# Performance work log

Hardware: AMD Instinct MI355X
Metric: run time of the kernel (lower is better)

## Reference

```python
import jax, jax.numpy as jnp
import numpy as np

HIDDEN = 64
DEPTH = 4  # 4 tanh layers + final linear


def _mlp(x, Ws, bs):
    # x: [..., 3] -> [..., 1]; weights stored as (in, out)
    h = x
    for W, b in zip(Ws[:-1], bs[:-1]):
        h = jnp.tanh(h @ W + b)
    return h @ Ws[-1] + bs[-1]


def setup_inputs() -> dict:
    key = jax.random.key(0)
    N = 262144
    dims = [3, HIDDEN, HIDDEN, HIDDEN, HIDDEN, 1]
    ks = jax.random.split(key, 2 * len(dims) + 3)
    inp = {}
    inp["x_data"] = jax.random.normal(ks[0], (N, 3), dtype=jnp.float32)
    inp["y_data"] = jax.random.normal(ks[1], (N, 1), dtype=jnp.float32)
    inp["x_phys"] = jax.random.normal(ks[2], (N, 3), dtype=jnp.float32)
    for i in range(5):
        fan_in = dims[i]
        bound = 1.0 / np.sqrt(fan_in)
        inp[f"W{i}"] = jax.random.uniform(ks[3 + 2 * i], (dims[i], dims[i + 1]),
                                          minval=-bound, maxval=bound, dtype=jnp.float32)
        inp[f"b{i}"] = jax.random.uniform(ks[4 + 2 * i], (dims[i + 1],),
                                          minval=-bound, maxval=bound, dtype=jnp.float32)
    inp["log_lambda"] = jnp.array([-2.0], dtype=jnp.float32)
    inp["log_alpha"] = jnp.array([-4.0], dtype=jnp.float32)
    return inp


def reference(x_data, y_data, x_phys,
              W0, b0, W1, b1, W2, b2, W3, b3, W4, b4,
              log_lambda, log_alpha):
    Ws = (W0, W1, W2, W3, W4)
    bs = (b0, b1, b2, b3, b4)
    alpha = jnp.exp(log_alpha)[0]
    lam = jnp.exp(log_lambda)[0]

    # data loss
    y_pred = _mlp(x_data, Ws, bs)  # [N,1]
    data_loss = jnp.mean((y_pred - y_data) ** 2)

    # PDE residual: dT/dt - alpha * (d2T/dx2 + d2T/dy2)
    def scalar_net(x):  # x: [3] -> scalar
        return _mlp(x, Ws, bs)[0]

    g = jax.grad(scalar_net)
    grads = jax.vmap(g)(x_phys)  # [N,3]
    dT_dt = grads[:, 2]

    e0 = jnp.array([1.0, 0.0, 0.0], dtype=x_phys.dtype)
    e1 = jnp.array([0.0, 1.0, 0.0], dtype=x_phys.dtype)

    def second_xy(x):
        # forward-over-reverse: Hessian columns for x and y directions
        _, hx = jax.jvp(g, (x,), (e0,))
        _, hy = jax.jvp(g, (x,), (e1,))
        return hx[0], hy[1]

    d2T_dx2, d2T_dy2 = jax.vmap(second_xy)(x_phys)  # each [N]

    residual = dT_dt - alpha * (d2T_dx2 + d2T_dy2)
    pde_loss = jnp.mean(residual ** 2)
    total_loss = data_loss + lam * pde_loss
    return total_loss, data_loss, pde_loss, alpha, lam
```

## Files before the change

### kernel.cpp

```cpp
#include <hip/hip_runtime.h>
#include <math.h>

#define NSAMP 262144
#define NW 8
#define BLK 512
#define GRID 1024
#define TOTW (GRID * NW)

#define SB_MASK 0x120

typedef _Float16 f16x8 __attribute__((ext_vector_type(8)));
typedef __fp16   fp16x2 __attribute__((ext_vector_type(2)));
typedef float    f32x4 __attribute__((ext_vector_type(4)));
typedef float    f32x2 __attribute__((ext_vector_type(2)));
typedef unsigned int u32;

#define PCH 4

#define TWO_LOG2E 2.8853900817779268f

union BFrag { f16x8 v[2]; u32 d[8]; };

__device__ __forceinline__ f32x2 lo2(f32x4 v) { return __builtin_shufflevector(v, v, 0, 1); }
__device__ __forceinline__ f32x2 hi2(f32x4 v) { return __builtin_shufflevector(v, v, 2, 3); }
__device__ __forceinline__ f32x2 splat2(float s) { f32x2 v; v.x = s; v.y = s; return v; }

__device__ __forceinline__ u32 pkdw(f32x2 p) {
    union { fp16x2 h; u32 u; } c;
    c.h = __builtin_amdgcn_cvt_pkrtz(p.x, p.y);
    return c.u;
}

__device__ __forceinline__ f32x2 fast_tanh2(f32x2 x) {
    f32x2 t = x * splat2(TWO_LOG2E);
    f32x2 e;
    e.x = __builtin_amdgcn_exp2f(t.x);
    e.y = __builtin_amdgcn_exp2f(t.y);
    f32x2 d = e + splat2(1.0f);
    f32x2 rc;
    rc.x = __builtin_amdgcn_rcpf(d.x);
    rc.y = __builtin_amdgcn_rcpf(d.y);
    return splat2(1.0f) - splat2(2.0f) * rc;
}

__device__ __forceinline__ void phys_half(f32x2 z0, f32x2 z1, f32x2 z2, f32x2 z3,
                                          f32x2 alpha2, f32x2 (&h)[PCH])
{
    f32x2 a    = fast_tanh2(z0);
    f32x2 ap   = splat2(1.0f) - a * a;
    f32x2 napp = (a * ap) * alpha2;
    h[0] = a;
    h[1] = ap * z1;
    h[2] = ap * z2;
    f32x2 s = z1 * z1 + z2 * z2;
    h[3] = ap * z3 + napp * s;
}

__device__ __forceinline__ f32x2 phys_resid(f32x2 z0, f32x2 z1, f32x2 z2, f32x2 z3,
                                            f32x2 alpha2)
{
    f32x2 a    = fast_tanh2(z0);
    f32x2 ap   = splat2(1.0f) - a * a;
    f32x2 napp = (a * ap) * alpha2;
    f32x2 s = z1 * z1 + z2 * z2;
    return ap * z3 + napp * s;
}

__device__ __forceinline__ double shfl_xor_d(double v, int m) {
    union { double d; int i[2]; } u; u.d = v;
    u.i[0] = __shfl_xor(u.i[0], m, 64);
    u.i[1] = __shfl_xor(u.i[1], m, 64);
    return u.d;
}

template<bool DATA, int CH>
__device__ __forceinline__ void pw_store(const f32x4* acc, BFrag (&bout)[CH],
                                         int rt, f32x2 alpha2)
{
    if constexpr (DATA) {
        #pragma unroll
        for (int c = 0; c < CH; c++) {
            bout[c].d[rt * 2 + 0] = pkdw(fast_tanh2(lo2(acc[c])));
            bout[c].d[rt * 2 + 1] = pkdw(fast_tanh2(hi2(acc[c])));
        }
    } else {
        f32x2 hlo[PCH], hhi[PCH];
        phys_half(lo2(acc[0]), lo2(acc[1]), lo2(acc[2]), lo2(acc[3]), alpha2, hlo);
        phys_half(hi2(acc[0]), hi2(acc[1]), hi2(acc[2]), hi2(acc[3]), alpha2, hhi);
        #pragma unroll
        for (int c = 0; c < CH; c++) {
            bout[c].d[rt * 2 + 0] = pkdw(hlo[c]);
            bout[c].d[rt * 2 + 1] = pkdw(hhi[c]);
        }
    }
}

template<bool DATA, int CH>
__device__ __forceinline__ void layer_mfma(
    const _Float16* sWA, const float (*sB)[64],
    int l, int rt, int q, int n, const BFrag (&bf)[CH], f32x4 (&acc)[CH])
{
    const f32x4 z4 = {0.f, 0.f, 0.f, 0.f};
    f16x8 a0k = *(const f16x8*)&sWA[((((l * 4 + rt) * 2 + 0) * 4 + q) * 16 + n) * 8];
    f16x8 a1k = *(const f16x8*)&sWA[((((l * 4 + rt) * 2 + 1) * 4 + q) * 16 + n) * 8];
    f32x4 bias = *(const f32x4*)&sB[l + 1][rt * 16 + q * 4];
    #pragma unroll
    for (int c = 0; c < CH; c++) {
        f32x4 cin = (DATA || c == 0) ? bias : z4;
        acc[c] = __builtin_amdgcn_mfma_f32_16x16x32_f16(a0k, bf[c].v[0], cin, 0, 0, 0);
        acc[c] = __builtin_amdgcn_mfma_f32_16x16x32_f16(a1k, bf[c].v[1], acc[c], 0, 0, 0);
    }
}

template<bool DATA, int CH>
__device__ __forceinline__ void hidden_layer(
    const _Float16* sWA, const float (*sB)[64],
    int l, int q, int n, const BFrag (&bin)[CH], BFrag (&bout)[CH], f32x2 alpha2)
{
    #pragma unroll
    for (int rt = 0; rt < 4; rt++) {
        f32x4 acc[CH];
        layer_mfma<DATA, CH>(sWA, sB, l, rt, q, n, bin, acc);
        pw_store<DATA, CH>(acc, bout, rt, alpha2);
        __builtin_amdgcn_sched_barrier(SB_MASK);
    }
}

template<bool DATA, int CH>
__device__ __forceinline__ double run_mode(
    const float* __restrict__ xd, const float* __restrict__ yd,
    const float* __restrict__ xp, float alpha,
    const _Float16* sWA, const f16x8 (&a0r)[4],
    const float (*sB)[64], const float (*sW0r)[64], const float* sW4, float b4,
    int q, int n, int wstart, int wstride)
{
    const f32x4 z4 = {0.f, 0.f, 0.f, 0.f};
    const f32x2 alpha2 = splat2(2.0f * alpha);

    const int SPI = DATA ? (16 * CH) : 16;
    const int NIT = NSAMP / SPI;
    double dacc = 0.0;

    const float* px = (DATA ? xd : xp) + (size_t)(wstart * SPI + n) * 3;
    const float* py = yd + (size_t)(wstart * SPI) + n;
    const size_t xstep = (size_t)wstride * SPI * 3;
    const size_t ystep = (size_t)wstride * SPI;

    for (int it = wstart; it < NIT; it += wstride) {
        BFrag bfA[CH], bfB[CH];
        {
            const int NBF = DATA ? CH : 1;
            f16x8 b0f[NBF];
            #pragma unroll
            for (int c = 0; c < NBF; c++) {
                union { f16x8 v; u32 dd[4]; _Float16 h[8]; } u;
                u.dd[0] = u.dd[1] = u.dd[2] = u.dd[3] = 0u;
                if (q == 0) {
                    const float* pc = px + c * 48;
                    u.h[0] = (_Float16)pc[0];
                    u.h[1] = (_Float16)pc[1];
                    u.h[2] = (_Float16)pc[2];
                }
                b0f[c] = u.v;
            }
            #pragma unroll
            for (int rt = 0; rt < 4; rt++) {
                f32x4 bias = *(const f32x4*)&sB[0][rt * 16 + q * 4];
                f32x4 acc[CH];
                if (DATA) {
                    #pragma unroll
                    for (int c = 0; c < CH; c++)
                        acc[c] = __builtin_amdgcn_mfma_f32_16x16x32_f16(a0r[rt], b0f[c], bias, 0, 0, 0);
                } else {
                    acc[0] = __builtin_amdgcn_mfma_f32_16x16x32_f16(a0r[rt], b0f[0], bias, 0, 0, 0);
                    acc[1] = *(const f32x4*)&sW0r[0][rt * 16 + q * 4];
                    acc[2] = *(const f32x4*)&sW0r[1][rt * 16 + q * 4];
                    acc[3] = *(const f32x4*)&sW0r[2][rt * 16 + q * 4];
                }
                pw_store<DATA, CH>(acc, bfA, rt, alpha2);
                __builtin_amdgcn_sched_barrier(SB_MASK);
            }
        }

        hidden_layer<DATA, CH>(sWA, sB, 0, q, n, bfA, bfB, alpha2);
        hidden_layer<DATA, CH>(sWA, sB, 1, q, n, bfB, bfA, alpha2);

        f32x2 t2[CH];
        #pragma unroll
        for (int c = 0; c < CH; c++) t2[c] = splat2(0.f);
        f32x2 tr2 = splat2(0.f);
        #pragma unroll
        for (int rt = 0; rt < 4; rt++) {
            f32x4 acc[CH];
            layer_mfma<DATA, CH>(sWA, sB, 2, rt, q, n, bfA, acc);
            f32x4 w4v = *(const f32x4*)&sW4[rt * 16 + q * 4];
            f32x2 wlo = lo2(w4v), whi = hi2(w4v);
            if (DATA) {
                #pragma unroll
                for (int c = 0; c < CH; c++) {
                    t2[c] = t2[c] + wlo * fast_tanh2(lo2(acc[c]));
                    t2[c] = t2[c] + whi * fast_tanh2(hi2(acc[c]));
                }
            } else {
                tr2 = tr2 + wlo * phys_resid(lo2(acc[0]), lo2(acc[1]), lo2(acc[2]), lo2(acc[3]), alpha2);
                tr2 = tr2 + whi * phys_resid(hi2(acc[0]), hi2(acc[1]), hi2(acc[2]), hi2(acc[3]), alpha2);
            }
        }

        if (DATA) {
            float t[CH];
            #pragma unroll
            for (int c = 0; c < CH; c++) {
                t[c] = t2[c].x + t2[c].y;
                t[c] += __shfl_xor(t[c], 16, 64);
                t[c] += __shfl_xor(t[c], 32, 64);
            }
            if (q == 0) {
                #pragma unroll
                for (int c = 0; c < CH; c++) {
                    float d = t[c] + b4 - py[c * 16];
                    dacc += (double)d * (double)d;
                }
            }
        } else {
            float tr = tr2.x + tr2.y;
            tr += __shfl_xor(tr, 16, 64);
            tr += __shfl_xor(tr, 32, 64);
            if (q == 0) dacc += (double)tr * (double)tr;
        }

        px += xstep;
        py += ystep;
    }
    return dacc;
}

__global__ __launch_bounds__(BLK)
__attribute__((amdgpu_waves_per_eu(2, 8)))
void fused_kernel(
    const float* __restrict__ xd, const float* __restrict__ yd, const float* __restrict__ xp,
    const float* __restrict__ W0, const float* __restrict__ b0,
    const float* __restrict__ W1, const float* __restrict__ b1,
    const float* __restrict__ W2, const float* __restrict__ b2,
    const float* __restrict__ W3, const float* __restrict__ b3,
    const float* __restrict__ W4, const float* __restrict__ b4,
    const float* __restrict__ log_alpha,
    double* __restrict__ accg)
{
    __shared__ __align__(16) _Float16 sWA[3 * 4 * 2 * 4 * 16 * 8];
    __shared__ __align__(16) float sB[4][64];
    __shared__ __align__(16) float sW0r[3][64];
    __shared__ __align__(16) float sW4s[64];
    __shared__ float sb4;
    __shared__ double sRedP[NW], sRedD[NW];

    const int tid = threadIdx.x;
    for (int idx = tid; idx < 3 * 4096; idx += BLK) {
        int l = idx >> 12, rem = idx & 4095, k = rem >> 6, m = rem & 63;
        const float* Ws = (l == 0) ? W1 : (l == 1) ? W2 : W3;
        int pk_ = (2 * (k >> 5) + ((k >> 2) & 1)) * 16 + ((k >> 3) & 3) * 4 + (k & 3);
        int rt = m >> 4, mlo = m & 15, kt = k >> 5, qq = (k >> 3) & 3, j = k & 7;
        sWA[((((l * 4 + rt) * 2 + kt) * 4 + qq) * 16 + mlo) * 8 + j] = (_Float16)Ws[pk_ * 64 + m];
    }
    for (int i = tid; i < 64; i += BLK) {
        sB[0][i] = b0[i]; sB[1][i] = b1[i]; sB[2][i] = b2[i]; sB[3][i] = b3[i];
        sW4s[i] = W4[i];
    }
    if (tid < 192) ((float*)sW0r)[tid] = (float)(_Float16)W0[tid];
    if (tid == 0) sb4 = b4[0];

    const int wave = tid >> 6, lane = tid & 63;
    const int q = lane >> 4, n = lane & 15;
    const float alpha = __expf(log_alpha[0]);

    f16x8 a0r[4];
    #pragma unroll
    for (int rt = 0; rt < 4; rt++) {
        f16x8 v = {0, 0, 0, 0, 0, 0, 0, 0};
        if (q == 0) {
            v[0] = (_Float16)W0[0 * 64 + rt * 16 + n];
            v[1] = (_Float16)W0[1 * 64 + rt * 16 + n];
            v[2] = (_Float16)W0[2 * 64 + rt * 16 + n];
        }
        a0r[rt] = v;
    }
    __syncthreads();

    const int wid = blockIdx.x * NW + wave;
    double dp = run_mode<false, 4>(xd, yd, xp, alpha, sWA, a0r, sB, sW0r, sW4s, sb4,
                                   q, n, wid, TOTW);
    double dd = run_mode<true, 2>(xd, yd, xp, alpha, sWA, a0r, sB, sW0r, sW4s, sb4,
                                  q, n, wid, TOTW);
    #pragma unroll
    for (int m = 1; m < 64; m <<= 1) {
        dp = dp + shfl_xor_d(dp, m);
        dd = dd + shfl_xor_d(dd, m);
    }
    if (lane == 0) { sRedP[wave] = dp; sRedD[wave] = dd; }
    __syncthreads();
    if (tid == 0) {
        double sp = 0.0, sd = 0.0;
        #pragma unroll
        for (int w = 0; w < NW; w++) { sp += sRedP[w]; sd += sRedD[w]; }
        accg[2 * blockIdx.x + 0] = sp;
        accg[2 * blockIdx.x + 1] = sd;
    }
}

__global__ void finalize_kernel(const double* __restrict__ ws,
                                const float* __restrict__ log_lambda,
                                const float* __restrict__ log_alpha,
                                float* __restrict__ out)
{
    __shared__ double sp[256], sd[256];
    int tid = threadIdx.x;
    double pd = 0.0, dd = 0.0;
    for (int i = tid; i < GRID; i += 256) {
        pd += ws[2 * i + 0];
        dd += ws[2 * i + 1];
    }
    sp[tid] = pd; sd[tid] = dd;
    __syncthreads();
    for (int s = 128; s > 0; s >>= 1) {
        if (tid < s) { sp[tid] += sp[tid + s]; sd[tid] += sd[tid + s]; }
        __syncthreads();
    }
    if (tid == 0) {
        float pde_loss  = (float)(sp[0] / (double)NSAMP);
        float data_loss = (float)(sd[0] / (double)NSAMP);
        float alpha = expf(log_alpha[0]);
        float lam   = expf(log_lambda[0]);
        out[0] = data_loss + lam * pde_loss;
        out[1] = data_loss;
        out[2] = pde_loss;
        out[3] = alpha;
        out[4] = lam;
    }
}

extern "C" void kernel_launch(void* const* d_in, const int* in_sizes, int n_in,
                              void* d_out, int out_size, void* d_ws, size_t ws_size,
                              hipStream_t stream) {
    const float* xd = (const float*)d_in[0];
    const float* yd = (const float*)d_in[1];
    const float* xp = (const float*)d_in[2];
    const float* W0 = (const float*)d_in[3];
    const float* b0 = (const float*)d_in[4];
    const float* W1 = (const float*)d_in[5];
    const float* b1 = (const float*)d_in[6];
    const float* W2 = (const float*)d_in[7];
    const float* b2 = (const float*)d_in[8];
    const float* W3 = (const float*)d_in[9];
    const float* b3 = (const float*)d_in[10];
    const float* W4 = (const float*)d_in[11];
    const float* b4 = (const float*)d_in[12];
    const float* log_lambda = (const float*)d_in[13];
    const float* log_alpha  = (const float*)d_in[14];
    float* out = (float*)d_out;
    double* acc = (double*)d_ws;

    fused_kernel<<<GRID, BLK, 0, stream>>>(xd, yd, xp, W0, b0, W1, b1, W2, b2, W3, b3,
                                           W4, b4, log_alpha, acc);
    finalize_kernel<<<1, 256, 0, stream>>>(acc, log_lambda, log_alpha, out);
}
```

Before: 151.1 us.

## Split waves into PDE-only and data-then-PDE groups to balance per-wave work

Instead of every wave running the full PDE pass and then the data pass, waves 0-3 handle the first 12288 PDE iterations. Waves 4-7 run the whole data pass and then the remaining 4096 PDE iterations. Each group strides over its own 4096-wave index space. The aim is to let the two modes run at the same time within a CU, mixing their different instruction profiles and balancing the work. The risk is load imbalance if the per-iteration costs of the two modes differ from what the fixed split assumes. The final reduction is spread across two threads.

```diff
diff --git a/kernel.cpp b/kernel.cpp
--- a/kernel.cpp
+++ b/kernel.cpp
@@ -5,7 +5,7 @@
 #define NW 8
 #define BLK 512
 #define GRID 1024
-#define TOTW (GRID * NW)
+#define HALFW 4096
 
 #define SB_MASK 0x120
 
@@ -132,13 +132,12 @@
     const float* __restrict__ xp, float alpha,
     const _Float16* sWA, const f16x8 (&a0r)[4],
     const float (*sB)[64], const float (*sW0r)[64], const float* sW4, float b4,
-    int q, int n, int wstart, int wstride)
+    int q, int n, int wstart, int wstride, int NIT)
 {
     const f32x4 z4 = {0.f, 0.f, 0.f, 0.f};
     const f32x2 alpha2 = splat2(2.0f * alpha);
 
-    const int SPI = DATA ? (16 * CH) : 16;
-    const int NIT = NSAMP / SPI;
+    constexpr int SPI = DATA ? (16 * CH) : 16;
     double dacc = 0.0;
 
     const float* px = (DATA ? xd : xp) + (size_t)(wstart * SPI + n) * 3;
@@ -149,7 +148,7 @@
     for (int it = wstart; it < NIT; it += wstride) {
         BFrag bfA[CH], bfB[CH];
         {
-            const int NBF = DATA ? CH : 1;
+            constexpr int NBF = DATA ? CH : 1;
             f16x8 b0f[NBF];
             #pragma unroll
             for (int c = 0; c < NBF; c++) {
@@ -286,11 +285,19 @@
     }
     __syncthreads();
 
-    const int wid = blockIdx.x * NW + wave;
-    double dp = run_mode<false, 4>(xd, yd, xp, alpha, sWA, a0r, sB, sW0r, sW4s, sb4,
-                                   q, n, wid, TOTW);
-    double dd = run_mode<true, 2>(xd, yd, xp, alpha, sWA, a0r, sB, sW0r, sW4s, sb4,
-                                  q, n, wid, TOTW);
+    double dp, dd;
+    if (wave < 4) {
+        int gpw = blockIdx.x * 4 + wave;
+        dp = run_mode<false, 4>(xd, yd, xp, alpha, sWA, a0r, sB, sW0r, sW4s, sb4,
+                                q, n, gpw, HALFW, 12288);
+        dd = 0.0;
+    } else {
+        int gdw = blockIdx.x * 4 + (wave - 4);
+        dd = run_mode<true, 2>(xd, yd, xp, alpha, sWA, a0r, sB, sW0r, sW4s, sb4,
+                               q, n, gdw, HALFW, 8192);
+        dp = run_mode<false, 4>(xd, yd, xp, alpha, sWA, a0r, sB, sW0r, sW4s, sb4,
+                                q, n, 12288 + gdw, HALFW, 16384);
+    }
     #pragma unroll
     for (int m = 1; m < 64; m <<= 1) {
         dp = dp + shfl_xor_d(dp, m);
@@ -299,10 +306,15 @@
     if (lane == 0) { sRedP[wave] = dp; sRedD[wave] = dd; }
     __syncthreads();
     if (tid == 0) {
-        double sp = 0.0, sd = 0.0;
-        #pragma unroll
-        for (int w = 0; w < NW; w++) { sp += sRedP[w]; sd += sRedD[w]; }
+        double sp = 0.0;
+        #pragma unroll
+        for (int w = 0; w < NW; w++) sp += sRedP[w];
         accg[2 * blockIdx.x + 0] = sp;
+    }
+    if (tid == 64) {
+        double sd = 0.0;
+        #pragma unroll
+        for (int w = 0; w < NW; w++) sd += sRedD[w];
         accg[2 * blockIdx.x + 1] = sd;
     }
 }
```

After: 149.0 us. About the same (-1.4%).
